# Kernel tuning notes

Hardware: AMD Instinct MI355X
Metric: run time of the kernel (lower is better)

The kernel has to match this reference:

```python
import jax, jax.numpy as jnp
import numpy as np

N = 100000
E = 1600000
HID = 128
EPS = 1e-8


def _linear_params(key, fan_in, fan_out, bias=True, gain=1.0):
    kw, kb = jax.random.split(key)
    bound = gain / np.sqrt(fan_in)
    W = jax.random.uniform(kw, (fan_in, fan_out), jnp.float32, -bound, bound)
    if bias:
        b = jax.random.uniform(kb, (fan_out,), jnp.float32, -bound, bound)
        return W, b
    return W


def setup_inputs() -> dict:
    key = jax.random.key(0)
    ks = jax.random.split(key, 12)
    h = jax.random.normal(ks[0], (N, HID), jnp.float32)
    coord = jax.random.normal(ks[1], (N, 3), jnp.float32)
    edge_index = jax.random.randint(ks[2], (2, E), 0, N, jnp.int64)
    # edge_mlp: Linear(2*HID+1 -> HID), SiLU, Linear(HID -> HID), SiLU
    We1, be1 = _linear_params(ks[3], 2 * HID + 1, HID)
    We2, be2 = _linear_params(ks[4], HID, HID)
    # node_mlp: Linear(2*HID -> HID), SiLU, Linear(HID -> HID)
    Wn1, bn1 = _linear_params(ks[5], 2 * HID, HID)
    Wn2, bn2 = _linear_params(ks[6], HID, HID)
    # coord_mlp: Linear(HID -> HID), SiLU, Linear(HID -> 1, no bias, xavier gain=0.001)
    Wc1, bc1 = _linear_params(ks[7], HID, HID)
    Wc2 = _linear_params(ks[8], HID, 1, bias=False, gain=0.001 * np.sqrt(6.0 * HID / (HID + 1)))
    return {
        "h": h, "edge_index": edge_index, "coord": coord,
        "We1": We1, "be1": be1, "We2": We2, "be2": be2,
        "Wn1": Wn1, "bn1": bn1, "Wn2": Wn2, "bn2": bn2,
        "Wc1": Wc1, "bc1": bc1, "Wc2": Wc2,
    }


def _egcl(h, edge_index, coord, We1, be1, We2, be2, Wn1, bn1, Wn2, bn2, Wc1, bc1, Wc2):
    row, col = edge_index[0], edge_index[1]
    n = h.shape[0]
    # coord2radial (normalize=True, detach on norm)
    coord_diff = coord[row] - coord[col]                       # [E,3]
    radial = jnp.sum(coord_diff ** 2, axis=1, keepdims=True)   # [E,1]
    norm = jax.lax.stop_gradient(jnp.sqrt(radial)) + EPS
    coord_diff = coord_diff / norm
    # edge_model (no edge_attr, no attention)
    edge_in = jnp.concatenate([h[row], h[col], radial], axis=1)  # [E, 2H+1]
    m = jax.nn.silu(edge_in @ We1 + be1)
    m = jax.nn.silu(m @ We2 + be2)                               # [E,H]
    # coord_model (coords_agg='mean', tanh=False)
    phi_x = jax.nn.silu(m @ Wc1 + bc1) @ Wc2                     # [E,1]
    trans = coord_diff * phi_x                                   # [E,3]
    agg_c = jax.ops.segment_sum(trans, row, num_segments=n)
    cnt = jax.ops.segment_sum(jnp.ones((trans.shape[0],), trans.dtype), row, num_segments=n)
    agg_c = agg_c / jnp.clip(cnt, 1.0, None)[:, None]
    coord_out = coord + agg_c
    # node_model (residual=True)
    agg_h = jax.ops.segment_sum(m, row, num_segments=n)          # [N,H]
    node_in = jnp.concatenate([h, agg_h], axis=1)
    out = jax.nn.silu(node_in @ Wn1 + bn1) @ Wn2 + bn2
    h_out = h + out
    return h_out, coord_out


def reference(h, edge_index, coord, We1, be1, We2, be2, Wn1, bn1, Wn2, bn2, Wc1, bc1, Wc2):
    return _egcl(h, edge_index, coord, We1, be1, We2, be2, Wn1, bn1, Wn2, bn2, Wc1, bc1, Wc2)
```

## Files before the change

kernel.cpp:

```cpp
#include <hip/hip_runtime.h>

#define NN 100000
#define NE 1600000
#define HD 128
#define EPSV 1e-8f
#define EB 64
#define LPAD 136

typedef unsigned short ushort_t;
typedef __attribute__((ext_vector_type(8))) short bf16x8;
typedef __attribute__((ext_vector_type(4))) float f32x4;

__device__ __forceinline__ float silu_f(float x) {
    return x * __builtin_amdgcn_rcpf(1.0f + __expf(-x));
}
__device__ __forceinline__ float b2f(unsigned short u) {
    union { unsigned int i; float f; } v; v.i = ((unsigned int)u) << 16; return v.f;
}
__device__ __forceinline__ unsigned short f2b(float f) {
    union { float f; unsigned int i; } v; v.f = f;
    unsigned int r = v.i + 0x7fff + ((v.i >> 16) & 1);
    return (unsigned short)(r >> 16);
}
__device__ __forceinline__ unsigned int cvt_pk_bf16(float lo, float hi) {
    unsigned int r;
    asm("v_cvt_pk_bf16_f32 %0, %1, %2" : "=v"(r) : "v"(lo), "v"(hi));
    return r;
}
__device__ __forceinline__ bf16x8 frag_from_f32(const float* p) {
    float4 a0 = *(const float4*)p;
    float4 a1 = *(const float4*)(p + 4);
    union { bf16x8 v; uint4 u; } r;
    r.u.x = cvt_pk_bf16(a0.x, a0.y); r.u.y = cvt_pk_bf16(a0.z, a0.w);
    r.u.z = cvt_pk_bf16(a1.x, a1.y); r.u.w = cvt_pk_bf16(a1.z, a1.w);
    return r.v;
}

extern "C" __global__ __launch_bounds__(256)
void k_prep_hist(const int* __restrict__ ei, int* __restrict__ deg,
                 const float* __restrict__ We2, const float* __restrict__ Wc1,
                 const float* __restrict__ We1, const float* __restrict__ Wn1,
                 const float* __restrict__ Wn2,
                 ushort_t* __restrict__ We2T, ushort_t* __restrict__ Wc1T,
                 ushort_t* __restrict__ WabT, ushort_t* __restrict__ Wn1T,
                 ushort_t* __restrict__ Wn2T)
{
    int id = blockIdx.x * 256 + threadIdx.x;
    atomicAdd(&deg[ei[id]], 1);
    if (id < 16384) {
        int n = id >> 7, k = id & 127;
        We2T[id] = f2b(We2[k * HD + n]);
    } else if (id < 32768) {
        int r = id - 16384; int n = r >> 7, k = r & 127;
        Wc1T[r] = f2b(Wc1[k * HD + n]);
    } else if (id < 65536) {
        int r = id - 32768; int j = r >> 7, k = r & 127;
        float v = (j < 128) ? We1[k * HD + j] : We1[(size_t)(128 + k) * HD + (j - 128)];
        WabT[r] = f2b(v);
    } else if (id < 98304) {
        int r = id - 65536; int j = r >> 8, k = r & 255;
        Wn1T[r] = f2b(Wn1[(size_t)k * HD + j]);
    } else if (id < 114688) {
        int r = id - 98304; int j = r >> 7, k = r & 127;
        Wn2T[r] = f2b(Wn2[k * HD + j]);
    }
}

extern "C" __global__ __launch_bounds__(1024)
void k_scan1(const int* __restrict__ deg, int* __restrict__ bsum)
{
    __shared__ int wsum[16];
    const int tid = threadIdx.x;
    const int lane = tid & 63, w = tid >> 6;
    int i = blockIdx.x * 1024 + tid;
    int v = (i < NN) ? deg[i] : 0;
#pragma unroll
    for (int off = 32; off > 0; off >>= 1) v += __shfl_xor(v, off, 64);
    if (lane == 0) wsum[w] = v;
    __syncthreads();
    if (tid == 0) {
        int s = 0;
#pragma unroll
        for (int k = 0; k < 16; k++) s += wsum[k];
        bsum[blockIdx.x] = s;
    }
}

extern "C" __global__ __launch_bounds__(1024)
void k_scan3(const int* __restrict__ deg, const int* __restrict__ bsum,
             int* __restrict__ cursor)
{
    __shared__ int wsum[16];
    __shared__ int boff_s;
    const int tid = threadIdx.x;
    const int lane = tid & 63, w = tid >> 6;
    int i = blockIdx.x * 1024 + tid;
    int v = (i < NN) ? deg[i] : 0;
    int s = v;
#pragma unroll
    for (int off = 1; off < 64; off <<= 1) {
        int t = __shfl_up(s, off, 64);
        if (lane >= off) s += t;
    }
    if (lane == 63) wsum[w] = s;
    if (w == 0) {
        int a = 0;
        for (int k = lane; k < blockIdx.x; k += 64) a += bsum[k];
#pragma unroll
        for (int off = 32; off > 0; off >>= 1) a += __shfl_xor(a, off, 64);
        if (lane == 0) boff_s = a;
    }
    __syncthreads();
    if (w == 0) {
        int ws = (lane < 16) ? wsum[lane] : 0;
#pragma unroll
        for (int off = 1; off < 16; off <<= 1) {
            int t = __shfl_up(ws, off, 64);
            if (lane >= off) ws += t;
        }
        if (lane < 16) wsum[lane] = ws;
    }
    __syncthreads();
    int excl = boff_s + ((w > 0) ? wsum[w - 1] : 0) + s - v;
    if (i < NN) cursor[i] = excl;
}

extern "C" __global__ __launch_bounds__(256)
void k_sortids(const int* __restrict__ ei, int* __restrict__ cursor,
               int2* __restrict__ rc)
{
    int e = blockIdx.x * 256 + threadIdx.x;
    int r = ei[e], c = ei[NE + e];
    int slot = atomicAdd(&cursor[r], 1);
    rc[slot] = make_int2(r, c);
}

extern "C" __global__ __launch_bounds__(256)
void k_ab(const float* __restrict__ h, const ushort_t* __restrict__ WabT,
          const float* __restrict__ be1,
          ushort_t* __restrict__ A, ushort_t* __restrict__ B)
{
    const int tid = threadIdx.x;
    const int n0 = blockIdx.x * 64;
    const int wave = tid >> 6, lane = tid & 63;
    const int lr = lane & 15, lg = lane >> 4;
    const int node = n0 + wave * 16 + lr;
    const int nsrc = (node < NN) ? node : (NN - 1);

    f32x4 acc[16];
#pragma unroll
    for (int nt = 0; nt < 16; nt++) acc[nt] = (f32x4){0.f, 0.f, 0.f, 0.f};
#pragma unroll
    for (int ks = 0; ks < 4; ks++) {
        bf16x8 hf8 = frag_from_f32(h + (size_t)nsrc * HD + ks * 32 + lg * 8);
#pragma unroll
        for (int nt = 0; nt < 16; nt++) {
            bf16x8 wf = *(const bf16x8*)(WabT + (size_t)(nt * 16 + lr) * HD + ks * 32 + lg * 8);
            acc[nt] = __builtin_amdgcn_mfma_f32_16x16x32_bf16(wf, hf8, acc[nt], 0, 0, 0);
        }
    }
    if (node < NN) {
#pragma unroll
        for (int nt = 0; nt < 16; nt++) {
            float4 bias = (nt < 8) ? ((const float4*)be1)[nt * 4 + lg]
                                   : (float4){0.f, 0.f, 0.f, 0.f};
            uint2 pk;
            pk.x = cvt_pk_bf16(acc[nt][0] + bias.x, acc[nt][1] + bias.y);
            pk.y = cvt_pk_bf16(acc[nt][2] + bias.z, acc[nt][3] + bias.w);
            if (nt < 8)
                *(uint2*)(A + (size_t)node * HD + nt * 16 + lg * 4) = pk;
            else
                *(uint2*)(B + (size_t)node * HD + (nt - 8) * 16 + lg * 4) = pk;
        }
    }
}

extern "C" __global__ __launch_bounds__(128, 4)
void k_edge(const int2* __restrict__ rc, const float* __restrict__ coord,
            const ushort_t* __restrict__ A, const ushort_t* __restrict__ B,
            const float* __restrict__ WeL, const float* __restrict__ be2,
            const ushort_t* __restrict__ We2T,
            const ushort_t* __restrict__ Wc1T,
            const float* __restrict__ bc1, const float* __restrict__ Wc2,
            float* __restrict__ agg_h, float* __restrict__ agg_c)
{
    __shared__ ushort_t m_lds[EB][LPAD] __attribute__((aligned(16)));
    __shared__ float cd_lds[EB][3];
    __shared__ int rows_s[EB];
    __shared__ float bias_lds[384] __attribute__((aligned(16)));
    __shared__ float wel_lds[128] __attribute__((aligned(16)));

    const int tid = threadIdx.x;
    const int e  = tid >> 1;
    const int hf = tid & 1;
    const int wave = tid >> 6, lane = tid & 63;
    const int lr = lane & 15, lg = lane >> 4;

    {
        int i = tid;
        bias_lds[i]       = be2[i];
        bias_lds[128 + i] = bc1[i];
        bias_lds[256 + i] = Wc2[i];
        wel_lds[i] = WeL[i];
    }
    int2 rce = rc[blockIdx.x * EB + e];
    const int row = rce.x, col = rce.y;

    float c0 = coord[(size_t)row * 3 + 0] - coord[(size_t)col * 3 + 0];
    float c1 = coord[(size_t)row * 3 + 1] - coord[(size_t)col * 3 + 1];
    float c2 = coord[(size_t)row * 3 + 2] - coord[(size_t)col * 3 + 2];
    float radial = c0 * c0 + c1 * c1 + c2 * c2;
    if (hf == 0) {
        rows_s[e] = row;
        float inv = __builtin_amdgcn_rcpf(sqrtf(radial) + EPSV);
        cd_lds[e][0] = c0 * inv; cd_lds[e][1] = c1 * inv; cd_lds[e][2] = c2 * inv;
    }
    __syncthreads();

    {
        const bf16x8* A8 = (const bf16x8*)(A + (size_t)row * HD + hf * 64);
        const bf16x8* B8 = (const bf16x8*)(B + (size_t)col * HD + hf * 64);
        const float4* WL4 = (const float4*)wel_lds + hf * 16;
#pragma unroll
        for (int i = 0; i < 8; i++) {
            bf16x8 av = A8[i], bv = B8[i];
            float4 w0 = WL4[2 * i], w1 = WL4[2 * i + 1];
            float v0 = silu_f(b2f((ushort_t)av[0]) + b2f((ushort_t)bv[0]) + radial * w0.x);
            float v1 = silu_f(b2f((ushort_t)av[1]) + b2f((ushort_t)bv[1]) + radial * w0.y);
            float v2 = silu_f(b2f((ushort_t)av[2]) + b2f((ushort_t)bv[2]) + radial * w0.z);
            float v3 = silu_f(b2f((ushort_t)av[3]) + b2f((ushort_t)bv[3]) + radial * w0.w);
            float v4 = silu_f(b2f((ushort_t)av[4]) + b2f((ushort_t)bv[4]) + radial * w1.x);
            float v5 = silu_f(b2f((ushort_t)av[5]) + b2f((ushort_t)bv[5]) + radial * w1.y);
            float v6 = silu_f(b2f((ushort_t)av[6]) + b2f((ushort_t)bv[6]) + radial * w1.z);
            float v7 = silu_f(b2f((ushort_t)av[7]) + b2f((ushort_t)bv[7]) + radial * w1.w);
            uint4 p;
            p.x = cvt_pk_bf16(v0, v1); p.y = cvt_pk_bf16(v2, v3);
            p.z = cvt_pk_bf16(v4, v5); p.w = cvt_pk_bf16(v6, v7);
            *(uint4*)&m_lds[e][hf * 64 + i * 8] = p;
        }
    }

    f32x4 acc[2][8];
#pragma unroll
    for (int mt = 0; mt < 2; mt++)
#pragma unroll
        for (int nt = 0; nt < 8; nt++) acc[mt][nt] = (f32x4){0.f, 0.f, 0.f, 0.f};
    __builtin_amdgcn_s_setprio(1);
#pragma unroll
    for (int ks = 0; ks < 4; ks++) {
        bf16x8 mf0 = *(const bf16x8*)&m_lds[wave * 32 + lr][ks * 32 + lg * 8];
        bf16x8 mf1 = *(const bf16x8*)&m_lds[wave * 32 + 16 + lr][ks * 32 + lg * 8];
#pragma unroll
        for (int nt = 0; nt < 8; nt++) {
            bf16x8 wf = *(const bf16x8*)(We2T + (size_t)(nt * 16 + lr) * HD + ks * 32 + lg * 8);
            acc[0][nt] = __builtin_amdgcn_mfma_f32_16x16x32_bf16(wf, mf0, acc[0][nt], 0, 0, 0);
            acc[1][nt] = __builtin_amdgcn_mfma_f32_16x16x32_bf16(wf, mf1, acc[1][nt], 0, 0, 0);
        }
    }
    __builtin_amdgcn_s_setprio(0);
#pragma unroll
    for (int nt = 0; nt < 8; nt++) {
        float4 be2v = *(const float4*)&bias_lds[nt * 16 + lg * 4];
#pragma unroll
        for (int mt = 0; mt < 2; mt++) {
            float v0 = silu_f(acc[mt][nt][0] + be2v.x);
            float v1 = silu_f(acc[mt][nt][1] + be2v.y);
            float v2 = silu_f(acc[mt][nt][2] + be2v.z);
            float v3 = silu_f(acc[mt][nt][3] + be2v.w);
            uint2 pk; pk.x = cvt_pk_bf16(v0, v1); pk.y = cvt_pk_bf16(v2, v3);
            *(uint2*)&m_lds[wave * 32 + mt * 16 + lr][nt * 16 + lg * 4] = pk;
        }
    }

#pragma unroll
    for (int mt = 0; mt < 2; mt++)
#pragma unroll
        for (int nt = 0; nt < 8; nt++) acc[mt][nt] = (f32x4){0.f, 0.f, 0.f, 0.f};
    __builtin_amdgcn_s_setprio(1);
#pragma unroll
    for (int ks = 0; ks < 4; ks++) {
        bf16x8 mf0 = *(const bf16x8*)&m_lds[wave * 32 + lr][ks * 32 + lg * 8];
        bf16x8 mf1 = *(const bf16x8*)&m_lds[wave * 32 + 16 + lr][ks * 32 + lg * 8];
#pragma unroll
        for (int nt = 0; nt < 8; nt++) {
            bf16x8 wf = *(const bf16x8*)(Wc1T + (size_t)(nt * 16 + lr) * HD + ks * 32 + lg * 8);
            acc[0][nt] = __builtin_amdgcn_mfma_f32_16x16x32_bf16(wf, mf0, acc[0][nt], 0, 0, 0);
            acc[1][nt] = __builtin_amdgcn_mfma_f32_16x16x32_bf16(wf, mf1, acc[1][nt], 0, 0, 0);
        }
    }
    __builtin_amdgcn_s_setprio(0);

    float ph0 = 0.f, ph1 = 0.f;
#pragma unroll
    for (int nt = 0; nt < 8; nt++) {
        float4 bc1v = *(const float4*)&bias_lds[128 + nt * 16 + lg * 4];
        float4 wc2v = *(const float4*)&bias_lds[256 + nt * 16 + lg * 4];
        ph0 += silu_f(acc[0][nt][0] + bc1v.x) * wc2v.x
             + silu_f(acc[0][nt][1] + bc1v.y) * wc2v.y
             + silu_f(acc[0][nt][2] + bc1v.z) * wc2v.z
             + silu_f(acc[0][nt][3] + bc1v.w) * wc2v.w;
        ph1 += silu_f(acc[1][nt][0] + bc1v.x) * wc2v.x
             + silu_f(acc[1][nt][1] + bc1v.y) * wc2v.y
             + silu_f(acc[1][nt][2] + bc1v.z) * wc2v.z
             + silu_f(acc[1][nt][3] + bc1v.w) * wc2v.w;
    }
    ph0 += __shfl_xor(ph0, 16, 64); ph0 += __shfl_xor(ph0, 32, 64);
    ph1 += __shfl_xor(ph1, 16, 64); ph1 += __shfl_xor(ph1, 32, 64);
    if (lg == 0) {
        int e0 = wave * 32 + lr, e1 = e0 + 16;
        cd_lds[e0][0] *= ph0; cd_lds[e0][1] *= ph0; cd_lds[e0][2] *= ph0;
        cd_lds[e1][0] *= ph1; cd_lds[e1][1] *= ph1; cd_lds[e1][2] *= ph1;
    }

    __syncthreads();

    {
        const int j = tid;
        float acc_r = 0.f;
        int cur = rows_s[0];
        for (int es = 0; es < EB; es++) {
            int r = rows_s[es];
            if (r != cur) {
                atomicAdd(&agg_h[(size_t)cur * HD + j], acc_r);
                acc_r = 0.f; cur = r;
            }
            acc_r += b2f(m_lds[es][j]);
        }
        atomicAdd(&agg_h[(size_t)cur * HD + j], acc_r);
    }
    if (wave == 0) {
        int c = lane >> 4, sub = lane & 15;
        if (c < 3) {
            const int es0 = sub * 4, es1 = es0 + 4;
            float acc_r = 0.f;
            int cur = rows_s[es0];
            for (int es = es0; es < es1; es++) {
                int r = rows_s[es];
                if (r != cur) {
                    atomicAdd(&agg_c[(size_t)cur * 3 + c], acc_r);
                    acc_r = 0.f; cur = r;
                }
                acc_r += cd_lds[es][c];
            }
            atomicAdd(&agg_c[(size_t)cur * 3 + c], acc_r);
        }
    }
}

extern "C" __global__ __launch_bounds__(256)
void k_node(const float* __restrict__ h, const ushort_t* __restrict__ Wn1T,
            const float* __restrict__ bn1, const ushort_t* __restrict__ Wn2T,
            const float* __restrict__ bn2, const float* __restrict__ coord,
            const int* __restrict__ deg,
            float* __restrict__ hout ,
            float* __restrict__ cout )
{
    __shared__ ushort_t us[64][LPAD] __attribute__((aligned(16)));
    const int tid = threadIdx.x;
    const int n0 = blockIdx.x * 64;
    const int wave = tid >> 6, lane = tid & 63;
    const int lr = lane & 15, lg = lane >> 4;
    const int node = n0 + wave * 16 + lr;
    const int nsrc = (node < NN) ? node : (NN - 1);

    f32x4 acc[8];
#pragma unroll
    for (int nt = 0; nt < 8; nt++) acc[nt] = (f32x4){0.f, 0.f, 0.f, 0.f};
#pragma unroll
    for (int ks = 0; ks < 8; ks++) {
        const float* src = (ks < 4) ? (h + (size_t)nsrc * HD + ks * 32 + lg * 8)
                                    : (hout + (size_t)nsrc * HD + (ks - 4) * 32 + lg * 8);
        bf16x8 cf = frag_from_f32(src);
#pragma unroll
        for (int nt = 0; nt < 8; nt++) {
            bf16x8 wf = *(const bf16x8*)(Wn1T + (size_t)(nt * 16 + lr) * 256 + ks * 32 + lg * 8);
            acc[nt] = __builtin_amdgcn_mfma_f32_16x16x32_bf16(wf, cf, acc[nt], 0, 0, 0);
        }
    }
#pragma unroll
    for (int nt = 0; nt < 8; nt++) {
        float4 b1 = ((const float4*)bn1)[nt * 4 + lg];
        float v0 = silu_f(acc[nt][0] + b1.x);
        float v1 = silu_f(acc[nt][1] + b1.y);
        float v2 = silu_f(acc[nt][2] + b1.z);
        float v3 = silu_f(acc[nt][3] + b1.w);
        uint2 pk; pk.x = cvt_pk_bf16(v0, v1); pk.y = cvt_pk_bf16(v2, v3);
        *(uint2*)&us[wave * 16 + lr][nt * 16 + lg * 4] = pk;
    }

    f32x4 acc2[8];
#pragma unroll
    for (int nt = 0; nt < 8; nt++) acc2[nt] = (f32x4){0.f, 0.f, 0.f, 0.f};
#pragma unroll
    for (int ks = 0; ks < 4; ks++) {
        bf16x8 uf = *(const bf16x8*)&us[wave * 16 + lr][ks * 32 + lg * 8];
#pragma unroll
        for (int nt = 0; nt < 8; nt++) {
            bf16x8 wf = *(const bf16x8*)(Wn2T + (size_t)(nt * 16 + lr) * HD + ks * 32 + lg * 8);
            acc2[nt] = __builtin_amdgcn_mfma_f32_16x16x32_bf16(wf, uf, acc2[nt], 0, 0, 0);
        }
    }
    if (node < NN) {
#pragma unroll
        for (int nt = 0; nt < 8; nt++) {
            float4 b2 = ((const float4*)bn2)[nt * 4 + lg];
            size_t idx = (size_t)node * HD + nt * 16 + lg * 4;
            float4 hv = *(const float4*)(h + idx);
            float4 o;
            o.x = hv.x + acc2[nt][0] + b2.x;
            o.y = hv.y + acc2[nt][1] + b2.y;
            o.z = hv.z + acc2[nt][2] + b2.z;
            o.w = hv.w + acc2[nt][3] + b2.w;
            *(float4*)(hout + idx) = o;
        }
        if (lg == 0) {
            float invc = __builtin_amdgcn_rcpf(fmaxf((float)deg[node], 1.0f));
#pragma unroll
            for (int i = 0; i < 3; i++) {
                size_t idx = (size_t)node * 3 + i;
                cout[idx] = coord[idx] + cout[idx] * invc;
            }
        }
    }
}

extern "C" void kernel_launch(void* const* d_in, const int* in_sizes, int n_in,
                              void* d_out, int out_size, void* d_ws, size_t ws_size,
                              hipStream_t stream)
{
    const float* h     = (const float*)d_in[0];
    const int*   ei    = (const int*)d_in[1];
    const float* coord = (const float*)d_in[2];
    const float* We1   = (const float*)d_in[3];
    const float* be1   = (const float*)d_in[4];
    const float* We2   = (const float*)d_in[5];
    const float* be2   = (const float*)d_in[6];
    const float* Wn1   = (const float*)d_in[7];
    const float* bn1   = (const float*)d_in[8];
    const float* Wn2   = (const float*)d_in[9];
    const float* bn2   = (const float*)d_in[10];
    const float* Wc1   = (const float*)d_in[11];
    const float* bc1   = (const float*)d_in[12];
    const float* Wc2   = (const float*)d_in[13];

    float* out   = (float*)d_out;
    float* agg_h = out;
    float* agg_c = out + (size_t)NN * HD;

    ushort_t* A    = (ushort_t*)d_ws;
    ushort_t* B    = A + (size_t)NN * HD;
    ushort_t* We2T = B + (size_t)NN * HD;
    ushort_t* Wc1T = We2T + 16384;
    ushort_t* WabT = Wc1T + 16384;
    ushort_t* Wn1T = WabT + 32768;
    ushort_t* Wn2T = Wn1T + 32768;
    int* deg    = (int*)(Wn2T + 16384);
    int* cursor = deg + NN;
    int* bsum   = cursor + NN;
    int2* rc    = (int2*)(bsum + 128);
    const float* WeL = We1 + (size_t)2 * HD * HD;

    const int scan_nb = (NN + 1023) / 1024;

    hipMemsetAsync(d_out, 0, (size_t)out_size * sizeof(float), stream);
    hipMemsetAsync(deg, 0, (size_t)NN * sizeof(int), stream);

    k_prep_hist<<<NE / 256, 256, 0, stream>>>(ei, deg, We2, Wc1, We1, Wn1, Wn2,
                                              We2T, Wc1T, WabT, Wn1T, Wn2T);
    k_ab<<<(NN + 63) / 64, 256, 0, stream>>>(h, WabT, be1, A, B);
    k_scan1<<<scan_nb, 1024, 0, stream>>>(deg, bsum);
    k_scan3<<<scan_nb, 1024, 0, stream>>>(deg, bsum, cursor);
    k_sortids<<<NE / 256, 256, 0, stream>>>(ei, cursor, rc);
    k_edge<<<NE / EB, 128, 0, stream>>>(rc, coord, A, B, WeL, be2,
                                        We2T, Wc1T, bc1, Wc2, agg_h, agg_c);
    k_node<<<(NN + 63) / 64, 256, 0, stream>>>(h, Wn1T, bn1, Wn2T, bn2, coord,
                                               deg, agg_h, agg_c);
}
```

Measured before the change: 897.9 us.

## Double edge-kernel block to 256 threads, splitting gather and scatter phases across waves

The edge kernel now launches 256 threads per 64-edge block. Four threads per edge do the gather/SiLU phase instead of two, which raises memory-level parallelism for the A/B row loads. Only the first two waves run the MFMA MLP, and the agg_h scatter is split so each half of the block handles 32 edges. The s_setprio hints are removed and an extra barrier is added. The two idle waves during the matmul phase and the larger per-block register footprint may lower occupancy. Splitting the scatter can also produce more atomics at segment boundaries.

```diff
diff --git a/kernel.cpp b/kernel.cpp
--- a/kernel.cpp
+++ b/kernel.cpp
@@ -175,7 +175,7 @@
     }
 }
 
-extern "C" __global__ __launch_bounds__(128, 4)
+extern "C" __global__ __launch_bounds__(256, 4)
 void k_edge(const int2* __restrict__ rc, const float* __restrict__ coord,
             const ushort_t* __restrict__ A, const ushort_t* __restrict__ B,
             const float* __restrict__ WeL, const float* __restrict__ be2,
@@ -191,18 +191,14 @@
     __shared__ float wel_lds[128] __attribute__((aligned(16)));
 
     const int tid = threadIdx.x;
-    const int e  = tid >> 1;
-    const int hf = tid & 1;
+    const int e  = tid >> 2;
+    const int q  = tid & 3;
     const int wave = tid >> 6, lane = tid & 63;
     const int lr = lane & 15, lg = lane >> 4;
 
-    {
-        int i = tid;
-        bias_lds[i]       = be2[i];
-        bias_lds[128 + i] = bc1[i];
-        bias_lds[256 + i] = Wc2[i];
-        wel_lds[i] = WeL[i];
-    }
+    if (tid < 128) { bias_lds[tid] = be2[tid]; bias_lds[256 + tid] = Wc2[tid]; }
+    else           { bias_lds[tid] = bc1[tid - 128]; wel_lds[tid - 128] = WeL[tid - 128]; }
+
     int2 rce = rc[blockIdx.x * EB + e];
     const int row = rce.x, col = rce.y;
 
@@ -210,7 +206,7 @@
     float c1 = coord[(size_t)row * 3 + 1] - coord[(size_t)col * 3 + 1];
     float c2 = coord[(size_t)row * 3 + 2] - coord[(size_t)col * 3 + 2];
     float radial = c0 * c0 + c1 * c1 + c2 * c2;
-    if (hf == 0) {
+    if (q == 0) {
         rows_s[e] = row;
         float inv = __builtin_amdgcn_rcpf(sqrtf(radial) + EPSV);
         cd_lds[e][0] = c0 * inv; cd_lds[e][1] = c1 * inv; cd_lds[e][2] = c2 * inv;
@@ -218,11 +214,11 @@
     __syncthreads();
 
     {
-        const bf16x8* A8 = (const bf16x8*)(A + (size_t)row * HD + hf * 64);
-        const bf16x8* B8 = (const bf16x8*)(B + (size_t)col * HD + hf * 64);
-        const float4* WL4 = (const float4*)wel_lds + hf * 16;
-#pragma unroll
-        for (int i = 0; i < 8; i++) {
+        const bf16x8* A8 = (const bf16x8*)(A + (size_t)row * HD + q * 32);
+        const bf16x8* B8 = (const bf16x8*)(B + (size_t)col * HD + q * 32);
+        const float4* WL4 = (const float4*)wel_lds + q * 8;
+#pragma unroll
+        for (int i = 0; i < 4; i++) {
             bf16x8 av = A8[i], bv = B8[i];
             float4 w0 = WL4[2 * i], w1 = WL4[2 * i + 1];
             float v0 = silu_f(b2f((ushort_t)av[0]) + b2f((ushort_t)bv[0]) + radial * w0.x);
@@ -236,89 +232,89 @@
             uint4 p;
             p.x = cvt_pk_bf16(v0, v1); p.y = cvt_pk_bf16(v2, v3);
             p.z = cvt_pk_bf16(v4, v5); p.w = cvt_pk_bf16(v6, v7);
-            *(uint4*)&m_lds[e][hf * 64 + i * 8] = p;
-        }
-    }
-
-    f32x4 acc[2][8];
-#pragma unroll
-    for (int mt = 0; mt < 2; mt++)
-#pragma unroll
-        for (int nt = 0; nt < 8; nt++) acc[mt][nt] = (f32x4){0.f, 0.f, 0.f, 0.f};
-    __builtin_amdgcn_s_setprio(1);
-#pragma unroll
-    for (int ks = 0; ks < 4; ks++) {
-        bf16x8 mf0 = *(const bf16x8*)&m_lds[wave * 32 + lr][ks * 32 + lg * 8];
-        bf16x8 mf1 = *(const bf16x8*)&m_lds[wave * 32 + 16 + lr][ks * 32 + lg * 8];
+            *(uint4*)&m_lds[e][q * 32 + i * 8] = p;
+        }
+    }
+    __syncthreads();
+
+    if (wave < 2) {
+        f32x4 acc[2][8];
+#pragma unroll
+        for (int mt = 0; mt < 2; mt++)
+#pragma unroll
+            for (int nt = 0; nt < 8; nt++) acc[mt][nt] = (f32x4){0.f, 0.f, 0.f, 0.f};
+#pragma unroll
+        for (int ks = 0; ks < 4; ks++) {
+            bf16x8 mf0 = *(const bf16x8*)&m_lds[wave * 32 + lr][ks * 32 + lg * 8];
+            bf16x8 mf1 = *(const bf16x8*)&m_lds[wave * 32 + 16 + lr][ks * 32 + lg * 8];
+#pragma unroll
+            for (int nt = 0; nt < 8; nt++) {
+                bf16x8 wf = *(const bf16x8*)(We2T + (size_t)(nt * 16 + lr) * HD + ks * 32 + lg * 8);
+                acc[0][nt] = __builtin_amdgcn_mfma_f32_16x16x32_bf16(wf, mf0, acc[0][nt], 0, 0, 0);
+                acc[1][nt] = __builtin_amdgcn_mfma_f32_16x16x32_bf16(wf, mf1, acc[1][nt], 0, 0, 0);
+            }
+        }
 #pragma unroll
         for (int nt = 0; nt < 8; nt++) {
-            bf16x8 wf = *(const bf16x8*)(We2T + (size_t)(nt * 16 + lr) * HD + ks * 32 + lg * 8);
-            acc[0][nt] = __builtin_amdgcn_mfma_f32_16x16x32_bf16(wf, mf0, acc[0][nt], 0, 0, 0);
-            acc[1][nt] = __builtin_amdgcn_mfma_f32_16x16x32_bf16(wf, mf1, acc[1][nt], 0, 0, 0);
-        }
-    }
-    __builtin_amdgcn_s_setprio(0);
-#pragma unroll
-    for (int nt = 0; nt < 8; nt++) {
-        float4 be2v = *(const float4*)&bias_lds[nt * 16 + lg * 4];
-#pragma unroll
-        for (int mt = 0; mt < 2; mt++) {
-            float v0 = silu_f(acc[mt][nt][0] + be2v.x);
-            float v1 = silu_f(acc[mt][nt][1] + be2v.y);
-            float v2 = silu_f(acc[mt][nt][2] + be2v.z);
-            float v3 = silu_f(acc[mt][nt][3] + be2v.w);
-            uint2 pk; pk.x = cvt_pk_bf16(v0, v1); pk.y = cvt_pk_bf16(v2, v3);
-            *(uint2*)&m_lds[wave * 32 + mt * 16 + lr][nt * 16 + lg * 4] = pk;
-        }
-    }
-
-#pragma unroll
-    for (int mt = 0; mt < 2; mt++)
-#pragma unroll
-        for (int nt = 0; nt < 8; nt++) acc[mt][nt] = (f32x4){0.f, 0.f, 0.f, 0.f};
-    __builtin_amdgcn_s_setprio(1);
-#pragma unroll
-    for (int ks = 0; ks < 4; ks++) {
-        bf16x8 mf0 = *(const bf16x8*)&m_lds[wave * 32 + lr][ks * 32 + lg * 8];
-        bf16x8 mf1 = *(const bf16x8*)&m_lds[wave * 32 + 16 + lr][ks * 32 + lg * 8];
+            float4 be2v = *(const float4*)&bias_lds[nt * 16 + lg * 4];
+#pragma unroll
+            for (int mt = 0; mt < 2; mt++) {
+                float v0 = silu_f(acc[mt][nt][0] + be2v.x);
+                float v1 = silu_f(acc[mt][nt][1] + be2v.y);
+                float v2 = silu_f(acc[mt][nt][2] + be2v.z);
+                float v3 = silu_f(acc[mt][nt][3] + be2v.w);
+                uint2 pk; pk.x = cvt_pk_bf16(v0, v1); pk.y = cvt_pk_bf16(v2, v3);
+                *(uint2*)&m_lds[wave * 32 + mt * 16 + lr][nt * 16 + lg * 4] = pk;
+            }
+        }
+
+#pragma unroll
+        for (int mt = 0; mt < 2; mt++)
+#pragma unroll
+            for (int nt = 0; nt < 8; nt++) acc[mt][nt] = (f32x4){0.f, 0.f, 0.f, 0.f};
+#pragma unroll
+        for (int ks = 0; ks < 4; ks++) {
+            bf16x8 mf0 = *(const bf16x8*)&m_lds[wave * 32 + lr][ks * 32 + lg * 8];
+            bf16x8 mf1 = *(const bf16x8*)&m_lds[wave * 32 + 16 + lr][ks * 32 + lg * 8];
+#pragma unroll
+            for (int nt = 0; nt < 8; nt++) {
+                bf16x8 wf = *(const bf16x8*)(Wc1T + (size_t)(nt * 16 + lr) * HD + ks * 32 + lg * 8);
+                acc[0][nt] = __builtin_amdgcn_mfma_f32_16x16x32_bf16(wf, mf0, acc[0][nt], 0, 0, 0);
+                acc[1][nt] = __builtin_amdgcn_mfma_f32_16x16x32_bf16(wf, mf1, acc[1][nt], 0, 0, 0);
+            }
+        }
+
+        float ph0 = 0.f, ph1 = 0.f;
 #pragma unroll
         for (int nt = 0; nt < 8; nt++) {
-            bf16x8 wf = *(const bf16x8*)(Wc1T + (size_t)(nt * 16 + lr) * HD + ks * 32 + lg * 8);
-            acc[0][nt] = __builtin_amdgcn_mfma_f32_16x16x32_bf16(wf, mf0, acc[0][nt], 0, 0, 0);
-            acc[1][nt] = __builtin_amdgcn_mfma_f32_16x16x32_bf16(wf, mf1, acc[1][nt], 0, 0, 0);
-        }
-    }
-    __builtin_amdgcn_s_setprio(0);
-
-    float ph0 = 0.f, ph1 = 0.f;
-#pragma unroll
-    for (int nt = 0; nt < 8; nt++) {
-        float4 bc1v = *(const float4*)&bias_lds[128 + nt * 16 + lg * 4];
-        float4 wc2v = *(const float4*)&bias_lds[256 + nt * 16 + lg * 4];
-        ph0 += silu_f(acc[0][nt][0] + bc1v.x) * wc2v.x
-             + silu_f(acc[0][nt][1] + bc1v.y) * wc2v.y
-             + silu_f(acc[0][nt][2] + bc1v.z) * wc2v.z
-             + silu_f(acc[0][nt][3] + bc1v.w) * wc2v.w;
-        ph1 += silu_f(acc[1][nt][0] + bc1v.x) * wc2v.x
-             + silu_f(acc[1][nt][1] + bc1v.y) * wc2v.y
-             + silu_f(acc[1][nt][2] + bc1v.z) * wc2v.z
-             + silu_f(acc[1][nt][3] + bc1v.w) * wc2v.w;
-    }
-    ph0 += __shfl_xor(ph0, 16, 64); ph0 += __shfl_xor(ph0, 32, 64);
-    ph1 += __shfl_xor(ph1, 16, 64); ph1 += __shfl_xor(ph1, 32, 64);
-    if (lg == 0) {
-        int e0 = wave * 32 + lr, e1 = e0 + 16;
-        cd_lds[e0][0] *= ph0; cd_lds[e0][1] *= ph0; cd_lds[e0][2] *= ph0;
-        cd_lds[e1][0] *= ph1; cd_lds[e1][1] *= ph1; cd_lds[e1][2] *= ph1;
+            float4 bc1v = *(const float4*)&bias_lds[128 + nt * 16 + lg * 4];
+            float4 wc2v = *(const float4*)&bias_lds[256 + nt * 16 + lg * 4];
+            ph0 += silu_f(acc[0][nt][0] + bc1v.x) * wc2v.x
+                 + silu_f(acc[0][nt][1] + bc1v.y) * wc2v.y
+                 + silu_f(acc[0][nt][2] + bc1v.z) * wc2v.z
+                 + silu_f(acc[0][nt][3] + bc1v.w) * wc2v.w;
+            ph1 += silu_f(acc[1][nt][0] + bc1v.x) * wc2v.x
+                 + silu_f(acc[1][nt][1] + bc1v.y) * wc2v.y
+                 + silu_f(acc[1][nt][2] + bc1v.z) * wc2v.z
+                 + silu_f(acc[1][nt][3] + bc1v.w) * wc2v.w;
+        }
+        ph0 += __shfl_xor(ph0, 16, 64); ph0 += __shfl_xor(ph0, 32, 64);
+        ph1 += __shfl_xor(ph1, 16, 64); ph1 += __shfl_xor(ph1, 32, 64);
+        if (lg == 0) {
+            int e0 = wave * 32 + lr, e1 = e0 + 16;
+            cd_lds[e0][0] *= ph0; cd_lds[e0][1] *= ph0; cd_lds[e0][2] *= ph0;
+            cd_lds[e1][0] *= ph1; cd_lds[e1][1] *= ph1; cd_lds[e1][2] *= ph1;
+        }
     }
 
     __syncthreads();
 
     {
-        const int j = tid;
+        const int j = tid & 127, g = tid >> 7;
+        const int es0 = g * 32, es1 = es0 + 32;
         float acc_r = 0.f;
-        int cur = rows_s[0];
-        for (int es = 0; es < EB; es++) {
+        int cur = rows_s[es0];
+        for (int es = es0; es < es1; es++) {
             int r = rows_s[es];
             if (r != cur) {
                 atomicAdd(&agg_h[(size_t)cur * HD + j], acc_r);
@@ -471,7 +467,7 @@
     k_scan1<<<scan_nb, 1024, 0, stream>>>(deg, bsum);
     k_scan3<<<scan_nb, 1024, 0, stream>>>(deg, bsum, cursor);
     k_sortids<<<NE / 256, 256, 0, stream>>>(ei, cursor, rc);
-    k_edge<<<NE / EB, 128, 0, stream>>>(rc, coord, A, B, WeL, be2,
+    k_edge<<<NE / EB, 256, 0, stream>>>(rc, coord, A, B, WeL, be2,
                                         We2T, Wc1T, bc1, Wc2, agg_h, agg_c);
     k_node<<<(NN + 63) / 64, 256, 0, stream>>>(h, Wn1T, bn1, Wn2T, bn2, coord,
                                                deg, agg_h, agg_c);
```

New measurement: 961.6 us. +7.1%, slower.
